# Kernel tuning notes

Hardware: AMD Instinct MI355X
Metric: run time of the kernel (lower is better)

The kernel has to match this reference:

```python
import jax, jax.numpy as jnp
import numpy as np

M_DIM = 128   # vec_dim m
L_BAS = 64    # bas_dim L
RANK = 8      # sliding window length
BATCH = 32
SEQ = 2048


def _make_bbasis(L, m):
    # Bbasis[k, i] = cos(2*pi*(k+1)/(i+2)), fixed buffer
    k = jnp.arange(L, dtype=jnp.float32)[:, None]
    i = jnp.arange(m, dtype=jnp.float32)[None, :]
    return jnp.cos(2.0 * jnp.pi * (k + 1.0) / (i + 2.0))


def setup_inputs() -> dict:
    key = jax.random.key(0)
    k1, k2 = jax.random.split(key)
    seq_batch = jax.random.normal(k1, (BATCH, SEQ, M_DIM), dtype=jnp.float32)
    M = jnp.eye(M_DIM, dtype=jnp.float32)                     # nn.init.eye_
    Acoeff = jax.random.uniform(k2, (M_DIM, L_BAS), dtype=jnp.float32,
                                minval=-0.1, maxval=0.1)      # uniform(-0.1, 0.1)
    Bbasis = _make_bbasis(L_BAS, M_DIM)
    return {"seq_batch": seq_batch, "M": M, "Acoeff": Acoeff, "Bbasis": Bbasis}


def reference(seq_batch, M, Acoeff, Bbasis):
    B, S, m = seq_batch.shape
    L = Acoeff.shape[1]
    Nw = S - RANK + 1  # number of sliding windows (linear mode, stride 1)

    # unfold-equivalent: gather contiguous windows [B, Nw, RANK, m]
    idx = jnp.arange(Nw)[:, None] + jnp.arange(RANK)[None, :]
    windows = seq_batch[:, idx, :]
    agg = windows.mean(axis=2)              # rank_op='avg' -> [B, Nw, m]
    agg = jnp.einsum('bwm,nm->bwn', agg, M)  # agg @ M.T (linear map)

    # position-indexed basis target: N(k)[i] = Acoeff[i, k%L] * Bbasis[k%L, i]
    kmod = jnp.arange(Nw) % L
    Nk = Acoeff.T[kmod] * Bbasis[kmod]       # [Nw, m]

    # mean squared deviation over all windows / dims
    D = jnp.mean((agg - Nk[None, :, :]) ** 2)
    return D
```

## Files before the change

kernel.cpp:

```cpp
#include <hip/hip_runtime.h>

#define BATCH   32
#define SEQ     2048
#define MDIM    128
#define LBAS    64
#define NW      2041
#define STRIP   16
#define NCHUNK  12
#define APAD    136

typedef __attribute__((ext_vector_type(8))) short  short8;
typedef __attribute__((ext_vector_type(4))) float  float4v;

__device__ __forceinline__ unsigned short f2bf(float f) {
    unsigned int u = __float_as_uint(f);
    return (unsigned short)((u + 0x7FFFu + ((u >> 16) & 1u)) >> 16);
}

__global__ __launch_bounds__(256)
void ndd_prep(const float* __restrict__ Mmat,
              const float* __restrict__ Acoeff,
              const float* __restrict__ Bbasis,
              unsigned short* __restrict__ Mb,
              float* __restrict__ nk)
{
    const int gid = blockIdx.x * 256 + threadIdx.x;
    if (gid < 2048) {
        const int n = gid >> 4;
        const int c = gid & 15;
        const float* src = Mmat + n * MDIM + c * 8;
        short8 v;
        #pragma unroll
        for (int j = 0; j < 8; ++j) v[j] = (short)f2bf(src[j]);
        *reinterpret_cast<short8*>(Mb + ((size_t)(c * MDIM + n)) * 8) = v;
    } else if (gid < 2048 + 8192) {
        const int e = gid - 2048;
        const int k = e >> 7;
        const int n = e & 127;
        nk[k * MDIM + n] = Acoeff[n * LBAS + k] * Bbasis[k * MDIM + n];
    }
}

__global__ __launch_bounds__(256, 2)
void ndd_main(const float* __restrict__ x,
              const unsigned short* __restrict__ Mb,
              const float* __restrict__ nk,
              float* __restrict__ partial)
{
    __shared__ __align__(16) float sRaw[4][NCHUNK * 256];
    __shared__ __align__(16) unsigned short sA[4][STRIP * APAD];

    const int tid  = threadIdx.x;
    const int lane = tid & 63;
    const int wave = tid >> 6;

    const int s  = blockIdx.x * 4 + wave;
    const int b  = s >> 7;
    const int st = s & 127;
    const int W0 = st * STRIP;

    float*          sRw = &sRaw[wave][0];
    unsigned short* sAw = &sA[wave][0];

    {
        const float* xb = x + (size_t)b * SEQ * MDIM;
        #pragma unroll
        for (int c = 0; c < NCHUNK; ++c) {
            int r0 = W0 + 2 * c;
            r0 = r0 > 2046 ? 2046 : r0;
            const float* g = xb + (size_t)r0 * MDIM + lane * 4;
            __builtin_amdgcn_global_load_lds(
                (const __attribute__((address_space(1))) void*)g,
                (__attribute__((address_space(3))) void*)&sRw[c * 256],
                16, 0, 0);
        }
    }
    __builtin_amdgcn_sched_barrier(0);
    __builtin_amdgcn_s_waitcnt(0x0f70);
    __builtin_amdgcn_sched_barrier(0);

    {
        const int m4 = lane & 31;
        const int h  = lane >> 5;
        const float4v* R = reinterpret_cast<const float4v*>(sRw);

        float4v rows[15];
        #pragma unroll
        for (int i = 0; i < 15; ++i)
            rows[i] = R[(h * 8 + i) * 32 + m4];

        float4v acc = ((rows[0] + rows[1]) + (rows[2] + rows[3])) +
                      ((rows[4] + rows[5]) + (rows[6] + rows[7]));
        #pragma unroll
        for (int j = 0; j < 8; ++j) {
            if (j) acc += rows[7 + j] - rows[j - 1];
            unsigned int lo = (unsigned)f2bf(acc.x * 0.125f) | ((unsigned)f2bf(acc.y * 0.125f) << 16);
            unsigned int hi = (unsigned)f2bf(acc.z * 0.125f) | ((unsigned)f2bf(acc.w * 0.125f) << 16);
            *reinterpret_cast<unsigned long long*>(&sAw[(h * 8 + j) * APAD + m4 * 4]) =
                ((unsigned long long)hi << 32) | lo;
        }
    }

    const int l15 = lane & 15;
    const int q   = lane >> 4;

    float4v accf[8];
    #pragma unroll
    for (int nt = 0; nt < 8; ++nt) accf[nt] = (float4v){0.f, 0.f, 0.f, 0.f};

    #pragma unroll
    for (int kk = 0; kk < 4; ++kk) {
        const short8 af = *reinterpret_cast<const short8*>(
            &sAw[l15 * APAD + kk * 32 + q * 8]);
        #pragma unroll
        for (int nt = 0; nt < 8; ++nt) {
            const short8 bf = *reinterpret_cast<const short8*>(
                Mb + ((size_t)((kk * 4 + q) * MDIM + nt * 16 + l15)) * 8);
            accf[nt] = __builtin_amdgcn_mfma_f32_16x16x32_bf16(af, bf, accf[nt], 0, 0, 0);
        }
    }

    const int kbase = W0 & 63;
    float local = 0.f;
    #pragma unroll
    for (int nt = 0; nt < 8; ++nt) {
        const int n = nt * 16 + l15;
        #pragma unroll
        for (int r = 0; r < 4; ++r) {
            const int w = q * 4 + r;
            if (W0 + w < NW) {
                const float v = nk[(kbase + w) * MDIM + n];
                const float d = accf[nt][r] - v;
                local += d * d;
            }
        }
    }
    #pragma unroll
    for (int off = 32; off > 0; off >>= 1)
        local += __shfl_down(local, off, 64);
    if (lane == 0) partial[s] = local;
}

__global__ __launch_bounds__(256)
void ndd_reduce(const float* __restrict__ partial, float* __restrict__ out)
{
    __shared__ float sred[4];
    float s = 0.f;
    #pragma unroll
    for (int i = 0; i < 16; ++i) s += partial[i * 256 + threadIdx.x];
    #pragma unroll
    for (int off = 32; off > 0; off >>= 1) s += __shfl_down(s, off, 64);
    if ((threadIdx.x & 63) == 0) sred[threadIdx.x >> 6] = s;
    __syncthreads();
    if (threadIdx.x == 0)
        out[0] = ((sred[0] + sred[1]) + (sred[2] + sred[3])) * (1.0f / 8359936.0f);
}

extern "C" void kernel_launch(void* const* d_in, const int* in_sizes, int n_in,
                              void* d_out, int out_size, void* d_ws, size_t ws_size,
                              hipStream_t stream) {
    const float* x     = (const float*)d_in[0];
    const float* Mmat  = (const float*)d_in[1];
    const float* Acoef = (const float*)d_in[2];
    const float* Bbas  = (const float*)d_in[3];
    float* out         = (float*)d_out;

    unsigned short* Mb = (unsigned short*)d_ws;
    float* nkp         = (float*)((char*)d_ws + 32768);
    float* part        = (float*)((char*)d_ws + 65536);

    ndd_prep<<<40, 256, 0, stream>>>(Mmat, Acoef, Bbas, Mb, nkp);
    ndd_main<<<1024, 256, 0, stream>>>(x, Mb, nkp, part);
    ndd_reduce<<<1, 256, 0, stream>>>(part, out);
}
```

Before: 94.94 us.

## Pipeline window tiles per block with triple-buffered LDS and register-resident M slices

Each block now handles 128 consecutive windows of one batch as 8 tiles of 16. A triple-buffered global_load_lds prefetch runs two tiles ahead, and all four waves cooperate on the sliding-window averaging while each wave owns 32 output columns. The wave's bf16 M fragments and nk targets are loaded into registers once instead of being refetched from global memory for every strip. The grid is halved, and partial sums are reduced within the block before the final kernel. This adds block-wide barriers and more register pressure, and gives fewer blocks to hide latency with.

Result: faster. 83.30 us (-12.3%).

```diff
diff --git a/kernel.cpp b/kernel.cpp
--- a/kernel.cpp
+++ b/kernel.cpp
@@ -5,8 +5,8 @@
 #define MDIM    128
 #define LBAS    64
 #define NW      2041
-#define STRIP   16
-#define NCHUNK  12
+#define TW      16
+#define NTILE   8
 #define APAD    136
 
 typedef __attribute__((ext_vector_type(8))) short  short8;
@@ -15,6 +15,11 @@
 __device__ __forceinline__ unsigned short f2bf(float f) {
     unsigned int u = __float_as_uint(f);
     return (unsigned short)((u + 0x7FFFu + ((u >> 16) & 1u)) >> 16);
+}
+__device__ __forceinline__ void store_bf16x4(unsigned short* p, float4v a) {
+    unsigned int lo = (unsigned)f2bf(a.x) | ((unsigned)f2bf(a.y) << 16);
+    unsigned int hi = (unsigned)f2bf(a.z) | ((unsigned)f2bf(a.w) << 16);
+    *reinterpret_cast<unsigned long long*>(p) = ((unsigned long long)hi << 32) | lo;
 }
 
 __global__ __launch_bounds__(256)
@@ -47,107 +52,125 @@
               const float* __restrict__ nk,
               float* __restrict__ partial)
 {
-    __shared__ __align__(16) float sRaw[4][NCHUNK * 256];
-    __shared__ __align__(16) unsigned short sA[4][STRIP * APAD];
+    __shared__ __align__(16) float sRaw[3][12 * 256];
+    __shared__ __align__(16) unsigned short sA[TW * APAD];
+    __shared__ float sred[4];
 
     const int tid  = threadIdx.x;
     const int lane = tid & 63;
     const int wave = tid >> 6;
+    const int b    = blockIdx.x >> 4;
+    const int base = (blockIdx.x & 15) * 128;
+    const float* xb = x + (size_t)b * SEQ * MDIM;
 
-    const int s  = blockIdx.x * 4 + wave;
-    const int b  = s >> 7;
-    const int st = s & 127;
-    const int W0 = st * STRIP;
+    const int l15 = lane & 15;
+    const int q   = lane >> 4;
+    const int nb  = wave * 32;
 
-    float*          sRw = &sRaw[wave][0];
-    unsigned short* sAw = &sA[wave][0];
+    short8 bfr[4][2];
+    #pragma unroll
+    for (int kk = 0; kk < 4; ++kk)
+        #pragma unroll
+        for (int nj = 0; nj < 2; ++nj)
+            bfr[kk][nj] = *reinterpret_cast<const short8*>(
+                Mb + ((size_t)((kk * 4 + q) * MDIM + nb + nj * 16 + l15)) * 8);
 
-    {
-        const float* xb = x + (size_t)b * SEQ * MDIM;
+    float nkreg[4][2][4];
+    #pragma unroll
+    for (int p = 0; p < 4; ++p)
         #pragma unroll
-        for (int c = 0; c < NCHUNK; ++c) {
-            int r0 = W0 + 2 * c;
+        for (int nj = 0; nj < 2; ++nj)
+            #pragma unroll
+            for (int r = 0; r < 4; ++r)
+                nkreg[p][nj][r] = nk[(p * 16 + q * 4 + r) * MDIM + nb + nj * 16 + l15];
+
+    auto issue = [&](int j) {
+        const int W0r = base + j * TW;
+        #pragma unroll
+        for (int i = 0; i < 3; ++i) {
+            const int c = wave * 3 + i;
+            int r0 = W0r + 2 * c;
             r0 = r0 > 2046 ? 2046 : r0;
             const float* g = xb + (size_t)r0 * MDIM + lane * 4;
             __builtin_amdgcn_global_load_lds(
                 (const __attribute__((address_space(1))) void*)g,
-                (__attribute__((address_space(3))) void*)&sRw[c * 256],
+                (__attribute__((address_space(3))) void*)&sRaw[j % 3][c * 256],
                 16, 0, 0);
         }
-    }
-    __builtin_amdgcn_sched_barrier(0);
-    __builtin_amdgcn_s_waitcnt(0x0f70);
-    __builtin_amdgcn_sched_barrier(0);
+    };
+    issue(0);
+    issue(1);
 
-    {
-        const int m4 = lane & 31;
-        const int h  = lane >> 5;
-        const float4v* R = reinterpret_cast<const float4v*>(sRw);
+    float local = 0.f;
 
-        float4v rows[15];
+    #pragma unroll
+    for (int j = 0; j < NTILE; ++j) {
+        __builtin_amdgcn_sched_barrier(0);
+        if (j == NTILE - 1) __builtin_amdgcn_s_waitcnt(0x0F70);
+        else                __builtin_amdgcn_s_waitcnt(0x0F73);
+        asm volatile("s_barrier" ::: "memory");
+        __builtin_amdgcn_sched_barrier(0);
+
+        {
+            const int m4 = tid & 31;
+            const int wg = tid >> 5;
+            const float4v* R = reinterpret_cast<const float4v*>(&sRaw[j % 3][0]);
+            float4v rows[9];
+            #pragma unroll
+            for (int i = 0; i < 9; ++i) rows[i] = R[(wg * 2 + i) * 32 + m4];
+            float4v acc = ((rows[0] + rows[1]) + (rows[2] + rows[3])) +
+                          ((rows[4] + rows[5]) + (rows[6] + rows[7]));
+            store_bf16x4(&sA[(wg * 2) * APAD + m4 * 4], acc * 0.125f);
+            acc += rows[8] - rows[0];
+            store_bf16x4(&sA[(wg * 2 + 1) * APAD + m4 * 4], acc * 0.125f);
+        }
+
+        __builtin_amdgcn_sched_barrier(0);
+        __builtin_amdgcn_s_waitcnt(0xC07F);
+        asm volatile("s_barrier" ::: "memory");
+        __builtin_amdgcn_sched_barrier(0);
+
+        if (j + 2 < NTILE) issue(j + 2);
+
+        float4v accf[2] = {(float4v){0.f,0.f,0.f,0.f}, (float4v){0.f,0.f,0.f,0.f}};
         #pragma unroll
-        for (int i = 0; i < 15; ++i)
-            rows[i] = R[(h * 8 + i) * 32 + m4];
+        for (int kk = 0; kk < 4; ++kk) {
+            const short8 af = *reinterpret_cast<const short8*>(
+                &sA[l15 * APAD + kk * 32 + q * 8]);
+            #pragma unroll
+            for (int nj = 0; nj < 2; ++nj)
+                accf[nj] = __builtin_amdgcn_mfma_f32_16x16x32_bf16(
+                    af, bfr[kk][nj], accf[nj], 0, 0, 0);
+        }
 
-        float4v acc = ((rows[0] + rows[1]) + (rows[2] + rows[3])) +
-                      ((rows[4] + rows[5]) + (rows[6] + rows[7]));
+        const int p = j & 3;
         #pragma unroll
-        for (int j = 0; j < 8; ++j) {
-            if (j) acc += rows[7 + j] - rows[j - 1];
-            unsigned int lo = (unsigned)f2bf(acc.x * 0.125f) | ((unsigned)f2bf(acc.y * 0.125f) << 16);
-            unsigned int hi = (unsigned)f2bf(acc.z * 0.125f) | ((unsigned)f2bf(acc.w * 0.125f) << 16);
-            *reinterpret_cast<unsigned long long*>(&sAw[(h * 8 + j) * APAD + m4 * 4]) =
-                ((unsigned long long)hi << 32) | lo;
+        for (int nj = 0; nj < 2; ++nj) {
+            #pragma unroll
+            for (int r = 0; r < 4; ++r) {
+                const int w = base + j * TW + q * 4 + r;
+                if (w < NW) {
+                    const float d = accf[nj][r] - nkreg[p][nj][r];
+                    local += d * d;
+                }
+            }
         }
     }
 
-    const int l15 = lane & 15;
-    const int q   = lane >> 4;
-
-    float4v accf[8];
-    #pragma unroll
-    for (int nt = 0; nt < 8; ++nt) accf[nt] = (float4v){0.f, 0.f, 0.f, 0.f};
-
-    #pragma unroll
-    for (int kk = 0; kk < 4; ++kk) {
-        const short8 af = *reinterpret_cast<const short8*>(
-            &sAw[l15 * APAD + kk * 32 + q * 8]);
-        #pragma unroll
-        for (int nt = 0; nt < 8; ++nt) {
-            const short8 bf = *reinterpret_cast<const short8*>(
-                Mb + ((size_t)((kk * 4 + q) * MDIM + nt * 16 + l15)) * 8);
-            accf[nt] = __builtin_amdgcn_mfma_f32_16x16x32_bf16(af, bf, accf[nt], 0, 0, 0);
-        }
-    }
-
-    const int kbase = W0 & 63;
-    float local = 0.f;
-    #pragma unroll
-    for (int nt = 0; nt < 8; ++nt) {
-        const int n = nt * 16 + l15;
-        #pragma unroll
-        for (int r = 0; r < 4; ++r) {
-            const int w = q * 4 + r;
-            if (W0 + w < NW) {
-                const float v = nk[(kbase + w) * MDIM + n];
-                const float d = accf[nt][r] - v;
-                local += d * d;
-            }
-        }
-    }
     #pragma unroll
     for (int off = 32; off > 0; off >>= 1)
         local += __shfl_down(local, off, 64);
-    if (lane == 0) partial[s] = local;
+    if (lane == 0) sred[wave] = local;
+    __syncthreads();
+    if (tid == 0)
+        partial[blockIdx.x] = (sred[0] + sred[1]) + (sred[2] + sred[3]);
 }
 
 __global__ __launch_bounds__(256)
 void ndd_reduce(const float* __restrict__ partial, float* __restrict__ out)
 {
     __shared__ float sred[4];
-    float s = 0.f;
-    #pragma unroll
-    for (int i = 0; i < 16; ++i) s += partial[i * 256 + threadIdx.x];
+    float s = partial[threadIdx.x] + partial[threadIdx.x + 256];
     #pragma unroll
     for (int off = 32; off > 0; off >>= 1) s += __shfl_down(s, off, 64);
     if ((threadIdx.x & 63) == 0) sred[threadIdx.x >> 6] = s;
@@ -170,6 +193,6 @@
     float* part        = (float*)((char*)d_ws + 65536);
 
     ndd_prep<<<40, 256, 0, stream>>>(Mmat, Acoef, Bbas, Mb, nkp);
-    ndd_main<<<1024, 256, 0, stream>>>(x, Mb, nkp, part);
+    ndd_main<<<512, 256, 0, stream>>>(x, Mb, nkp, part);
     ndd_reduce<<<1, 256, 0, stream>>>(part, out);
 }
```
